# Optimization experiments

Measured on AMD Instinct MI355X. Metric: run time of the kernel, lower is better.

Reference implementation:

```python
import jax, jax.numpy as jnp
import numpy as np

N = 50000
NUM_GRAPHS = 64
EPS = 1e-16  # PyG softmax denominator epsilon


def _gat_conv(x, src, dst, W, a_src, a_dst, b, heads, out_ch):
    n = x.shape[0]
    h = (x @ W).reshape(n, heads, out_ch)                    # [N,H,C]
    al_s = jnp.einsum('nhc,hc->nh', h, a_src)                # [N,H]
    al_d = jnp.einsum('nhc,hc->nh', h, a_dst)                # [N,H]
    e = jax.nn.leaky_relu(al_s[src] + al_d[dst], 0.2)        # [E,H]
    emax = jax.ops.segment_max(e, dst, num_segments=n)       # [N,H]
    ee = jnp.exp(e - emax[dst])
    den = jax.ops.segment_sum(ee, dst, num_segments=n)       # [N,H]
    alpha = ee / (den[dst] + EPS)                            # [E,H]
    msg = h[src] * alpha[:, :, None]                         # [E,H,C]
    out = jax.ops.segment_sum(msg, dst, num_segments=n)      # [N,H,C]
    return out.reshape(n, heads * out_ch) + b


def setup_inputs() -> dict:
    key = jax.random.key(0)
    ks = jax.random.split(key, 16)
    E = 250000
    x = jax.random.normal(ks[0], (N, 11), dtype=jnp.float32)
    edge_index = jax.random.randint(ks[1], (2, E), 0, N, dtype=jnp.int64)
    batch = jnp.sort(jax.random.randint(ks[2], (N,), 0, NUM_GRAPHS, dtype=jnp.int64))
    def glorot(k, shape):
        fan = shape[0] + shape[-1]
        return jax.random.uniform(k, shape, jnp.float32, -1.0, 1.0) * np.sqrt(6.0 / fan)
    return {
        'x': x, 'edge_index': edge_index, 'batch': batch,
        'W1': glorot(ks[3], (11, 8 * 128)),
        'a1s': glorot(ks[4], (8, 128)), 'a1d': glorot(ks[5], (8, 128)),
        'b1': jnp.zeros((8 * 128,), jnp.float32),
        'W2': glorot(ks[6], (1024, 8 * 64)),
        'a2s': glorot(ks[7], (8, 64)), 'a2d': glorot(ks[8], (8, 64)),
        'b2': jnp.zeros((8 * 64,), jnp.float32),
        'W3': glorot(ks[9], (512, 4 * 32)),
        'a3s': glorot(ks[10], (4, 32)), 'a3d': glorot(ks[11], (4, 32)),
        'b3': jnp.zeros((4 * 32,), jnp.float32),
        'Wout': glorot(ks[12], (128, 1)),
        'bout': jnp.zeros((1,), jnp.float32),
    }


def reference(x, edge_index, batch, W1, a1s, a1d, b1, W2, a2s, a2d, b2,
              W3, a3s, a3d, b3, Wout, bout):
    n = x.shape[0]
    # GATConv adds self-loops by default
    loop = jnp.arange(n, dtype=edge_index.dtype)
    src = jnp.concatenate([edge_index[0], loop])
    dst = jnp.concatenate([edge_index[1], loop])
    h = jax.nn.leaky_relu(_gat_conv(x, src, dst, W1, a1s, a1d, b1, 8, 128), 0.01)
    h = jax.nn.leaky_relu(_gat_conv(h, src, dst, W2, a2s, a2d, b2, 8, 64), 0.01)
    h = jax.nn.leaky_relu(_gat_conv(h, src, dst, W3, a3s, a3d, b3, 4, 32), 0.01)
    # global mean pool over graphs
    sums = jax.ops.segment_sum(h, batch, num_segments=NUM_GRAPHS)      # [G,128]
    cnt = jax.ops.segment_sum(jnp.ones((n,), h.dtype), batch, num_segments=NUM_GRAPHS)
    pooled = sums / jnp.maximum(cnt, 1.0)[:, None]
    return pooled @ Wout + bout                                        # [G,1]
```

## Files before the change

### kernel.cpp

```cpp
#include <hip/hip_runtime.h>

#define EPS 1e-16f

typedef __attribute__((ext_vector_type(8))) short short8;
typedef __attribute__((ext_vector_type(4))) float f32x4;

__device__ __forceinline__ float b2f(unsigned short u) {
    return __uint_as_float(((unsigned)u) << 16);
}
__device__ __forceinline__ unsigned short f2b(float f) {
    unsigned u = __float_as_uint(f);
    u += 0x7fffu + ((u >> 16) & 1u);
    return (unsigned short)(u >> 16);
}

typedef __attribute__((address_space(3))) void lds_vp;
typedef __attribute__((address_space(1))) const void glb_vp;
__device__ __forceinline__ void load_lds16(const unsigned short* g,
                                           unsigned short* l) {
    __builtin_amdgcn_global_load_lds((glb_vp*)g, (lds_vp*)l, 16, 0, 0);
}

__global__ void init_deg_kernel(int* deg, int N) {
    int i = blockIdx.x * blockDim.x + threadIdx.x;
    if (i < N) deg[i] = 1;
}

__global__ void hist_kernel(const int* __restrict__ ei, int E, int N, int* deg) {
    int e = blockIdx.x * blockDim.x + threadIdx.x;
    if (e < E) {
        int d = ei[E + e];
        if ((unsigned)d < (unsigned)N) atomicAdd(&deg[d], 1);
    }
}

__global__ void scan_block_kernel(const int* __restrict__ deg,
                                  int* __restrict__ rowst,
                                  int* __restrict__ bsum, int N) {
    __shared__ int s[256];
    int t = threadIdx.x, b = blockIdx.x;
    int i = b * 256 + t;
    s[t] = (i < N) ? deg[i] : 0;
    __syncthreads();
    for (int o = 1; o < 256; o <<= 1) {
        int a = (t >= o) ? s[t - o] : 0;
        __syncthreads();
        s[t] += a;
        __syncthreads();
    }
    if (i < N) rowst[i + 1] = s[t];
    if (t == 255) bsum[b] = s[255];
}

__global__ void scan_top_kernel(const int* __restrict__ bsum,
                                int* __restrict__ boff, int NB) {
    __shared__ int psum[65];
    int t = threadIdx.x;
    int chunk = (NB + 63) / 64;
    int lo = t * chunk, hi = lo + chunk;
    if (lo > NB) lo = NB;
    if (hi > NB) hi = NB;
    int s = 0;
    for (int i = lo; i < hi; i++) s += bsum[i];
    psum[t + 1] = s;
    __syncthreads();
    if (t == 0) {
        psum[0] = 0;
        for (int i = 1; i <= 64; i++) psum[i] += psum[i - 1];
    }
    __syncthreads();
    int run = psum[t];
    for (int i = lo; i < hi; i++) {
        boff[i] = run;
        run += bsum[i];
    }
}

__global__ void scan_add_kernel(int* __restrict__ rowst,
                                const int* __restrict__ boff, int N) {
    int i = blockIdx.x * 256 + threadIdx.x;
    if (i == 0) rowst[0] = 0;
    if (i < N) rowst[i + 1] += boff[blockIdx.x];
}

__global__ void selfloop_kernel(const int* __restrict__ rowst, int* srcs,
                                int* cursor, int N) {
    int n = blockIdx.x * blockDim.x + threadIdx.x;
    if (n < N) {
        srcs[rowst[n]] = n;
        cursor[n] = rowst[n] + 1;
    }
}

__global__ void scatter_kernel(const int* __restrict__ ei, int E, int N,
                               int* cursor, int* srcs) {
    int e = blockIdx.x * blockDim.x + threadIdx.x;
    if (e < E) {
        int d = ei[E + e];
        if ((unsigned)d < (unsigned)N) {
            int p = atomicAdd(&cursor[d], 1);
            int s = ei[e];
            if ((unsigned)s >= (unsigned)N) s = d;
            srcs[p] = s;
        }
    }
}

__global__ void wa1_kernel(const float* __restrict__ W1,
                           const float* __restrict__ a1s,
                           const float* __restrict__ a1d,
                           float* __restrict__ w_as, float* __restrict__ w_ad) {
    int t = threadIdx.x;
    if (t >= 88) return;
    int h = t / 11, k = t % 11;
    float s = 0.f, d = 0.f;
    for (int c = 0; c < 128; c++) {
        float w = W1[k * 1024 + h * 128 + c];
        s += w * a1s[h * 128 + c];
        d += w * a1d[h * 128 + c];
    }
    w_as[h * 16 + k] = s;
    w_ad[h * 16 + k] = d;
}

__global__ void al1_kernel(const float* __restrict__ x,
                           const float* __restrict__ w_as,
                           const float* __restrict__ w_ad,
                           float* __restrict__ als, float* __restrict__ ald,
                           int N) {
    int i = blockIdx.x * blockDim.x + threadIdx.x;
    if (i >= N * 8) return;
    int n = i >> 3, h = i & 7;
    float s = 0.f, d = 0.f;
#pragma unroll
    for (int k = 0; k < 11; k++) {
        float xv = x[n * 11 + k];
        s += xv * w_as[h * 16 + k];
        d += xv * w_ad[h * 16 + k];
    }
    als[i] = s;
    ald[i] = d;
}

__global__ void aggx_kernel(const float* __restrict__ x,
                            const float* __restrict__ escr,
                            const int* __restrict__ rowst,
                            const int* __restrict__ srcs,
                            unsigned short* __restrict__ A2, int N) {
    int n = blockIdx.x;
    int t = threadIdx.x;
    int h = t >> 4, k = t & 15;
    int start = rowst[n], end = rowst[n + 1];
    float acc = 0.f;
    const int CH = 4;
    for (int idx = start; idx < end; idx += CH) {
        int mc = end - idx;
        if (mc > CH) mc = CH;
        int ss[CH];
        float av[CH], xv[CH];
#pragma unroll
        for (int j = 0; j < CH; j++)
            if (j < mc) ss[j] = srcs[idx + j];
#pragma unroll
        for (int j = 0; j < CH; j++)
            if (j < mc) av[j] = escr[(size_t)(idx + j) * 8 + h];
#pragma unroll
        for (int j = 0; j < CH; j++)
            if (j < mc) xv[j] = (k < 11) ? x[ss[j] * 11 + k] : 0.f;
#pragma unroll
        for (int j = 0; j < CH; j++)
            if (j < mc) acc += av[j] * xv[j];
    }
    A2[(size_t)n * 128 + t] = f2b(acc);
}

__global__ void w1bd_kernel(const float* __restrict__ W1,
                            unsigned short* __restrict__ Bt) {
    int i = blockIdx.x * blockDim.x + threadIdx.x;
    if (i >= 1024 * 128) return;
    int n = i >> 7, kk = i & 127;
    int h = kk >> 4, k = kk & 15;
    float v = (h == (n >> 7) && k < 11) ? W1[k * 1024 + n] : 0.f;
    Bt[i] = f2b(v);
}

__global__ void transpose_w_kernel(const float* __restrict__ W,
                                   unsigned short* __restrict__ Wt, int K, int N) {
    int i = blockIdx.x * blockDim.x + threadIdx.x;
    if (i >= K * N) return;
    int k = i / N, n = i % N;
    Wt[(size_t)n * K + k] = f2b(W[i]);
}

template <bool EPI, int HB, int CC>
__global__ __launch_bounds__(256) void gemm_mfma(
    const unsigned short* __restrict__ A, const unsigned short* __restrict__ Bt,
    unsigned short* __restrict__ C, const float* __restrict__ bias,
    const float* __restrict__ a_s, const float* __restrict__ a_d,
    float* __restrict__ als, float* __restrict__ ald, int H, int M, int N,
    int K) {
    int NX = gridDim.x;
    int bid = blockIdx.y * NX + blockIdx.x;
    int win = bid & (8 * NX - 1);
    int mg = bid / (8 * NX);
    int m_t = mg * 8 + (win & 7);
    int n_t = win >> 3;
    int bm = m_t * 128, bn = n_t * 128;
    if (bm >= M) return;

    union SMem {
        struct {
            unsigned short As[2][128 * 32];
            unsigned short Bs[2][128 * 32];
        } k;
        unsigned short Ct[128 * 132];
    };
    __shared__ __align__(16) SMem sm;
    auto& As = sm.k.As;
    auto& Bs = sm.k.Bs;
    auto& Ct = sm.Ct;

    int t = threadIdx.x;
    int w = t >> 6, lane = t & 63;
    int quad = lane >> 4, l16 = lane & 15;
    int wr = (w >> 1) * 64, wc = (w & 1) * 64;

    int c0 = w * 128 + lane;
    int c1 = c0 + 64;
    int r0 = c0 >> 2, p0 = c0 & 3;
    int r1 = c1 >> 2, p1 = c1 & 3;
    int j0 = (p0 - (r0 >> 1)) & 3;
    int j1 = (p1 - (r1 >> 1)) & 3;
    int ga0 = bm + r0;
    if (ga0 >= M) ga0 = M - 1;
    int ga1 = bm + r1;
    if (ga1 >= M) ga1 = M - 1;
    const unsigned short* Ag0 = A + (size_t)ga0 * K + j0 * 8;
    const unsigned short* Ag1 = A + (size_t)ga1 * K + j1 * 8;
    const unsigned short* Bg0 = Bt + (size_t)(bn + r0) * K + j0 * 8;
    const unsigned short* Bg1 = Bt + (size_t)(bn + r1) * K + j1 * 8;

    auto stage = [&](int st, int k0) {
        load_lds16(Ag0 + k0, &As[st][(w * 128) * 8]);
        load_lds16(Ag1 + k0, &As[st][(w * 128 + 64) * 8]);
        load_lds16(Bg0 + k0, &Bs[st][(w * 128) * 8]);
        load_lds16(Bg1 + k0, &Bs[st][(w * 128 + 64) * 8]);
    };

    int aoff[4], boff4[4];
#pragma unroll
    for (int i = 0; i < 4; i++) {
        int ra = wr + i * 16 + l16;
        aoff[i] = ra * 32 + (((quad + (ra >> 1)) & 3) * 8);
        int rb = wc + i * 16 + l16;
        boff4[i] = rb * 32 + (((quad + (rb >> 1)) & 3) * 8);
    }

    f32x4 acc[4][4] = {};
    stage(0, 0);
    int st = 0;
    for (int k0 = 0; k0 < K; k0 += 32, st ^= 1) {
        __syncthreads();
        if (k0 + 32 < K) stage(st ^ 1, k0 + 32);
        short8 a[4], b[4];
#pragma unroll
        for (int mi = 0; mi < 4; mi++) a[mi] = *(const short8*)&As[st][aoff[mi]];
#pragma unroll
        for (int ni = 0; ni < 4; ni++) b[ni] = *(const short8*)&Bs[st][boff4[ni]];
#pragma unroll
        for (int mi = 0; mi < 4; mi++)
#pragma unroll
            for (int ni = 0; ni < 4; ni++)
                acc[mi][ni] = __builtin_amdgcn_mfma_f32_16x16x32_bf16(
                    a[mi], b[ni], acc[mi][ni], 0, 0, 0);
    }
    __syncthreads();

#pragma unroll
    for (int mi = 0; mi < 4; mi++) {
#pragma unroll
        for (int r = 0; r < 4; r++) {
            int rl = wr + mi * 16 + quad * 4 + r;
#pragma unroll
            for (int ni = 0; ni < 4; ni++) {
                int cl = wc + ni * 16 + l16;
                float v = acc[mi][ni][r];
                if (EPI) {
                    v += bias[bn + cl];
                    v = v > 0.f ? v : 0.01f * v;
                }
                Ct[rl * 132 + cl] = f2b(v);
            }
        }
    }
    __syncthreads();
#pragma unroll
    for (int p = 0; p < 16; p++) {
        int q = p * 256 + t;
        int row = q >> 5, c8 = q & 31;
        if (bm + row < M) {
            uint2 v = *(const uint2*)&Ct[row * 132 + c8 * 4];
            *(uint2*)&C[(size_t)(bm + row) * N + bn + c8 * 4] = v;
        }
    }
    if (HB > 0) {
        for (int pi = t; pi < 128 * HB; pi += 256) {
            int row = pi / HB, hl = pi % HB;
            if (bm + row >= M) continue;
            int hg = bn / CC + hl;
            const unsigned short* rp = &Ct[row * 132 + hl * CC];
            const float* asp = a_s + hg * CC;
            const float* adp = a_d + hg * CC;
            float s = 0.f, d = 0.f;
#pragma unroll
            for (int c = 0; c < CC; c++) {
                float v = b2f(rp[c]);
                s += v * asp[c];
                d += v * adp[c];
            }
            als[(size_t)(bm + row) * H + hg] = s;
            ald[(size_t)(bm + row) * H + hg] = d;
        }
    }
}

template <int H>
__global__ void mden_kernel(const float* __restrict__ als,
                            const float* __restrict__ ald,
                            const int* __restrict__ rowst,
                            const int* __restrict__ srcs,
                            float* __restrict__ escr, int N) {
    int i = blockIdx.x * blockDim.x + threadIdx.x;
    if (i >= N * H) return;
    int n = i / H, h = i % H;
    float aldn = ald[i];
    int start = rowst[n], end = rowst[n + 1];
    const int CH = 4;
    float m = -1e30f;
    for (int idx = start; idx < end; idx += CH) {
        int mc = end - idx;
        if (mc > CH) mc = CH;
        int ss[CH];
        float lv[CH];
#pragma unroll
        for (int j = 0; j < CH; j++)
            if (j < mc) ss[j] = srcs[idx + j];
#pragma unroll
        for (int j = 0; j < CH; j++)
            if (j < mc) lv[j] = als[ss[j] * H + h];
#pragma unroll
        for (int j = 0; j < CH; j++)
            if (j < mc) {
                float v = lv[j] + aldn;
                v = v > 0.f ? v : 0.2f * v;
                escr[(size_t)(idx + j) * H + h] = v;
                m = fmaxf(m, v);
            }
    }
    float den = 0.f;
    for (int idx = start; idx < end; idx += CH) {
        int mc = end - idx;
        if (mc > CH) mc = CH;
        float lv[CH];
#pragma unroll
        for (int j = 0; j < CH; j++)
            if (j < mc) lv[j] = escr[(size_t)(idx + j) * H + h];
#pragma unroll
        for (int j = 0; j < CH; j++)
            if (j < mc) den += expf(lv[j] - m);
    }
    float dinv = 1.0f / (den + EPS);
    for (int idx = start; idx < end; idx += CH) {
        int mc = end - idx;
        if (mc > CH) mc = CH;
        float lv[CH];
#pragma unroll
        for (int j = 0; j < CH; j++)
            if (j < mc) lv[j] = escr[(size_t)(idx + j) * H + h];
#pragma unroll
        for (int j = 0; j < CH; j++)
            if (j < mc)
                escr[(size_t)(idx + j) * H + h] = expf(lv[j] - m) * dinv;
    }
}

template <int H, int C>
__global__ void agg_fused4(const unsigned short* __restrict__ hin,
                           const float* __restrict__ als,
                           const float* __restrict__ ald,
                           const int* __restrict__ rowst,
                           const int* __restrict__ srcs,
                           const float* __restrict__ bias,
                           unsigned short* __restrict__ out, int N) {
    constexpr int HC = H * C;
    constexpr int TPH = C / 4;
    int n = blockIdx.x;
    int t = threadIdx.x;
    int c = t * 4;
    int hh = c / C;
    int li = (c % C) / 4;
    int start = rowst[n], end = rowst[n + 1];
    float aldn = ald[n * H + hh];
    float m = -1e30f;
    for (int idx = start + li; idx < end; idx += TPH) {
        float v = als[srcs[idx] * H + hh] + aldn;
        v = v > 0.f ? v : 0.2f * v;
        m = fmaxf(m, v);
    }
#pragma unroll
    for (int o = 1; o < TPH; o <<= 1) m = fmaxf(m, __shfl_xor(m, o));
    float den = 0.f;
    for (int idx = start + li; idx < end; idx += TPH) {
        float v = als[srcs[idx] * H + hh] + aldn;
        v = v > 0.f ? v : 0.2f * v;
        den += expf(v - m);
    }
#pragma unroll
    for (int o = 1; o < TPH; o <<= 1) den += __shfl_xor(den, o);
    float dinv = 1.0f / (den + EPS);

    float a0 = 0.f, a1 = 0.f, a2 = 0.f, a3 = 0.f;
    const int CH = 4;
    for (int idx = start; idx < end; idx += CH) {
        int mc = end - idx;
        if (mc > CH) mc = CH;
        int ss[CH];
        float lv[CH];
        ushort4 uv[CH];
#pragma unroll
        for (int j = 0; j < CH; j++)
            if (j < mc) ss[j] = srcs[idx + j];
#pragma unroll
        for (int j = 0; j < CH; j++)
            if (j < mc) lv[j] = als[ss[j] * H + hh];
#pragma unroll
        for (int j = 0; j < CH; j++)
            if (j < mc) uv[j] = *(const ushort4*)(hin + (size_t)ss[j] * HC + c);
#pragma unroll
        for (int j = 0; j < CH; j++)
            if (j < mc) {
                float v = lv[j] + aldn;
                v = v > 0.f ? v : 0.2f * v;
                float a = expf(v - m) * dinv;
                a0 += a * b2f(uv[j].x);
                a1 += a * b2f(uv[j].y);
                a2 += a * b2f(uv[j].z);
                a3 += a * b2f(uv[j].w);
            }
    }
    float v0 = a0 + bias[c], v1 = a1 + bias[c + 1];
    float v2 = a2 + bias[c + 2], v3 = a3 + bias[c + 3];
    ushort4 o;
    o.x = f2b(v0 > 0.f ? v0 : 0.01f * v0);
    o.y = f2b(v1 > 0.f ? v1 : 0.01f * v1);
    o.z = f2b(v2 > 0.f ? v2 : 0.01f * v2);
    o.w = f2b(v3 > 0.f ? v3 : 0.01f * v3);
    *(ushort4*)&out[(size_t)n * HC + c] = o;
}

template <int H, int C>
__global__ void agg_fused2(const unsigned short* __restrict__ hin,
                           const float* __restrict__ als,
                           const float* __restrict__ ald,
                           const int* __restrict__ rowst,
                           const int* __restrict__ srcs,
                           const float* __restrict__ bias,
                           unsigned short* __restrict__ out, int N) {
    constexpr int HC = H * C;
    constexpr int TPH = C / 2;
    int n = blockIdx.x;
    int t = threadIdx.x;
    int c = t * 2;
    int hh = c / C;
    int li = (c % C) / 2;
    int start = rowst[n], end = rowst[n + 1];
    float aldn = ald[n * H + hh];
    float m = -1e30f;
    for (int idx = start + li; idx < end; idx += TPH) {
        float v = als[srcs[idx] * H + hh] + aldn;
        v = v > 0.f ? v : 0.2f * v;
        m = fmaxf(m, v);
    }
#pragma unroll
    for (int o = 1; o < TPH; o <<= 1) m = fmaxf(m, __shfl_xor(m, o));
    float den = 0.f;
    for (int idx = start + li; idx < end; idx += TPH) {
        float v = als[srcs[idx] * H + hh] + aldn;
        v = v > 0.f ? v : 0.2f * v;
        den += expf(v - m);
    }
#pragma unroll
    for (int o = 1; o < TPH; o <<= 1) den += __shfl_xor(den, o);
    float dinv = 1.0f / (den + EPS);

    float a0 = 0.f, a1 = 0.f;
    const int CH = 4;
    for (int idx = start; idx < end; idx += CH) {
        int mc = end - idx;
        if (mc > CH) mc = CH;
        int ss[CH];
        float lv[CH];
        ushort2 uv[CH];
#pragma unroll
        for (int j = 0; j < CH; j++)
            if (j < mc) ss[j] = srcs[idx + j];
#pragma unroll
        for (int j = 0; j < CH; j++)
            if (j < mc) lv[j] = als[ss[j] * H + hh];
#pragma unroll
        for (int j = 0; j < CH; j++)
            if (j < mc) uv[j] = *(const ushort2*)(hin + (size_t)ss[j] * HC + c);
#pragma unroll
        for (int j = 0; j < CH; j++)
            if (j < mc) {
                float v = lv[j] + aldn;
                v = v > 0.f ? v : 0.2f * v;
                float a = expf(v - m) * dinv;
                a0 += a * b2f(uv[j].x);
                a1 += a * b2f(uv[j].y);
            }
    }
    float v0 = a0 + bias[c], v1 = a1 + bias[c + 1];
    ushort2 o;
    o.x = f2b(v0 > 0.f ? v0 : 0.01f * v0);
    o.y = f2b(v1 > 0.f ? v1 : 0.01f * v1);
    *(ushort2*)&out[(size_t)n * HC + c] = o;
}

__global__ void pool_init_kernel(float* pool, int GC) {
    int i = blockIdx.x * blockDim.x + threadIdx.x;
    if (i < GC) pool[i] = 0.f;
}

__global__ void pool_partial_kernel(const unsigned short* __restrict__ h3,
                                    const int* __restrict__ batch,
                                    float* __restrict__ pool, int N, int G) {
    int lo = blockIdx.x * 128;
    int hi = lo + 128;
    if (hi > N) hi = N;
    if (lo >= N) return;
    int t = threadIdx.x;
    int cur = batch[lo];
    float acc = 0.f;
    for (int n = lo; n < hi; n++) {
        int g = batch[n];
        if (g != cur) {
            if ((unsigned)cur < (unsigned)G) atomicAdd(&pool[cur * 128 + t], acc);
            acc = 0.f;
            cur = g;
        }
        acc += b2f(h3[(size_t)n * 128 + t]);
    }
    if ((unsigned)cur < (unsigned)G) atomicAdd(&pool[cur * 128 + t], acc);
}

__global__ void head_kernel(const float* __restrict__ pool,
                            const int* __restrict__ batch,
                            const float* __restrict__ Wout,
                            const float* __restrict__ bout,
                            float* __restrict__ out, int N) {
    int g = blockIdx.x;
    int t = threadIdx.x;
    int lo, hi;
    {
        int a = 0, b = N;
        while (a < b) { int mid = (a + b) >> 1; if (batch[mid] < g) a = mid + 1; else b = mid; }
        lo = a;
        a = lo; b = N;
        while (a < b) { int mid = (a + b) >> 1; if (batch[mid] < g + 1) a = mid + 1; else b = mid; }
        hi = a;
    }
    float c = (float)(hi - lo);
    c = c > 1.f ? c : 1.f;
    float v = (pool[g * 128 + t] / c) * Wout[t];
    for (int o = 32; o; o >>= 1) v += __shfl_xor(v, o);
    __shared__ float partial[2];
    if ((t & 63) == 0) partial[t >> 6] = v;
    __syncthreads();
    if (t == 0) out[g] = partial[0] + partial[1] + bout[0];
}

extern "C" void kernel_launch(void* const* d_in, const int* in_sizes, int n_in,
                              void* d_out, int out_size, void* d_ws,
                              size_t ws_size, hipStream_t stream) {
    const float* x = (const float*)d_in[0];
    const int* ei = (const int*)d_in[1];
    const int* batch = (const int*)d_in[2];
    const float* W1 = (const float*)d_in[3];
    const float* a1s = (const float*)d_in[4];
    const float* a1d = (const float*)d_in[5];
    const float* b1 = (const float*)d_in[6];
    const float* W2 = (const float*)d_in[7];
    const float* a2s = (const float*)d_in[8];
    const float* a2d = (const float*)d_in[9];
    const float* b2 = (const float*)d_in[10];
    const float* W3 = (const float*)d_in[11];
    const float* a3s = (const float*)d_in[12];
    const float* a3d = (const float*)d_in[13];
    const float* b3 = (const float*)d_in[14];
    const float* Wout = (const float*)d_in[15];
    const float* bout = (const float*)d_in[16];
    float* out = (float*)d_out;

    const int N = in_sizes[0] / 11;
    const int E = in_sizes[1] / 2;
    const int Etot = E + N;
    const int G = out_size;
    const int NB = (N + 255) / 256;
    const int MT = ((N + 127) / 128 + 7) / 8 * 8;

    char* ws = (char*)d_ws;
    size_t off = 0;
    auto alloc = [&](size_t bytes) -> void* {
        void* p = ws + off;
        off += (bytes + 255) & ~(size_t)255;
        return p;
    };
    unsigned short* buf1 = (unsigned short*)alloc((size_t)N * 1024 * 2);
    unsigned short* buf2 = (unsigned short*)alloc((size_t)N * 1024 * 2);
    float* als = (float*)alloc((size_t)N * 8 * 4);
    float* ald = (float*)alloc((size_t)N * 8 * 4);
    float* escr = (float*)alloc((size_t)Etot * 8 * 4);
    int* rowst = (int*)alloc((size_t)(N + 1) * 4);
    int* cursor = (int*)alloc((size_t)N * 4);
    int* srcs = (int*)alloc((size_t)Etot * 4);
    int* deg = (int*)alloc((size_t)N * 4);
    int* bsum = (int*)alloc((size_t)NB * 4);
    int* boff = (int*)alloc((size_t)NB * 4);
    float* pool = (float*)alloc((size_t)G * 128 * 4);
    unsigned short* aggx = (unsigned short*)alloc((size_t)N * 128 * 2);
    unsigned short* w1bd = (unsigned short*)alloc((size_t)1024 * 128 * 2);
    unsigned short* wt2 = (unsigned short*)alloc((size_t)1024 * 512 * 2);
    unsigned short* wt3 = (unsigned short*)alloc((size_t)512 * 128 * 2);
    float* w_as = (float*)alloc(8 * 16 * 4);
    float* w_ad = (float*)alloc(8 * 16 * 4);

    int nb = (N + 255) / 256;
    int eb = (E + 255) / 256;

    init_deg_kernel<<<nb, 256, 0, stream>>>(deg, N);
    hist_kernel<<<eb, 256, 0, stream>>>(ei, E, N, deg);
    scan_block_kernel<<<NB, 256, 0, stream>>>(deg, rowst, bsum, N);
    scan_top_kernel<<<1, 64, 0, stream>>>(bsum, boff, NB);
    scan_add_kernel<<<NB, 256, 0, stream>>>(rowst, boff, N);
    selfloop_kernel<<<nb, 256, 0, stream>>>(rowst, srcs, cursor, N);
    scatter_kernel<<<eb, 256, 0, stream>>>(ei, E, N, cursor, srcs);

    wa1_kernel<<<1, 128, 0, stream>>>(W1, a1s, a1d, w_as, w_ad);
    w1bd_kernel<<<(1024 * 128 + 255) / 256, 256, 0, stream>>>(W1, w1bd);
    transpose_w_kernel<<<(1024 * 512 + 255) / 256, 256, 0, stream>>>(W2, wt2,
                                                                     1024, 512);
    transpose_w_kernel<<<(512 * 128 + 255) / 256, 256, 0, stream>>>(W3, wt3,
                                                                    512, 128);

    al1_kernel<<<(N * 8 + 255) / 256, 256, 0, stream>>>(x, w_as, w_ad, als, ald,
                                                        N);
    mden_kernel<8><<<(N * 8 + 255) / 256, 256, 0, stream>>>(als, ald, rowst,
                                                            srcs, escr, N);
    aggx_kernel<<<N, 128, 0, stream>>>(x, escr, rowst, srcs, aggx, N);
    gemm_mfma<true, 0, 1><<<dim3(8, MT), 256, 0, stream>>>(
        aggx, w1bd, buf2, b1, nullptr, nullptr, nullptr, nullptr, 0, N, 1024,
        128);

    gemm_mfma<false, 2, 64><<<dim3(4, MT), 256, 0, stream>>>(
        buf2, wt2, buf1, nullptr, a2s, a2d, als, ald, 8, N, 512, 1024);
    agg_fused4<8, 64><<<N, 128, 0, stream>>>(buf1, als, ald, rowst, srcs, b2,
                                             buf2, N);

    gemm_mfma<false, 4, 32><<<dim3(1, MT), 256, 0, stream>>>(
        buf2, wt3, buf1, nullptr, a3s, a3d, als, ald, 4, N, 128, 512);
    agg_fused2<4, 32><<<N, 64, 0, stream>>>(buf1, als, ald, rowst, srcs, b3,
                                            buf2, N);

    pool_init_kernel<<<(G * 128 + 255) / 256, 256, 0, stream>>>(pool, G * 128);
    pool_partial_kernel<<<(N + 127) / 128, 128, 0, stream>>>(buf2, batch, pool,
                                                             N, G);
    head_kernel<<<G, 128, 0, stream>>>(pool, batch, Wout, bout, out, N);
}
```

Measured before the change: 491.6 us.

## Fuse preprocessing kernels and exploit block-diagonal W1 to shrink layer-1 GEMM K

After: 512.3 us. +4.2%, slower.

```diff
diff --git a/kernel.cpp b/kernel.cpp
--- a/kernel.cpp
+++ b/kernel.cpp
@@ -76,19 +76,19 @@
     }
 }
 
-__global__ void scan_add_kernel(int* __restrict__ rowst,
-                                const int* __restrict__ boff, int N) {
+__global__ void scan_finish_kernel(int* __restrict__ rowst,
+                                   const int* __restrict__ boff,
+                                   const int* __restrict__ deg,
+                                   int* __restrict__ srcs,
+                                   int* __restrict__ cursor, int N) {
     int i = blockIdx.x * 256 + threadIdx.x;
     if (i == 0) rowst[0] = 0;
-    if (i < N) rowst[i + 1] += boff[blockIdx.x];
-}
-
-__global__ void selfloop_kernel(const int* __restrict__ rowst, int* srcs,
-                                int* cursor, int N) {
-    int n = blockIdx.x * blockDim.x + threadIdx.x;
-    if (n < N) {
-        srcs[rowst[n]] = n;
-        cursor[n] = rowst[n] + 1;
+    if (i < N) {
+        int incl = rowst[i + 1] + boff[blockIdx.x];
+        rowst[i + 1] = incl;
+        int st = incl - deg[i];
+        srcs[st] = i;
+        cursor[i] = st + 1;
     }
 }
 
@@ -106,44 +106,69 @@
     }
 }
 
-__global__ void wa1_kernel(const float* __restrict__ W1,
+__global__ void wprep_kernel(const float* __restrict__ W1,
+                             const float* __restrict__ W2,
+                             const float* __restrict__ W3,
+                             unsigned short* __restrict__ wt2,
+                             unsigned short* __restrict__ wt3,
+                             unsigned short* __restrict__ w1sk) {
+    int i = blockIdx.x * blockDim.x + threadIdx.x;
+    if (i < 1024 * 512) {
+        int k = i / 512, n = i % 512;
+        wt2[(size_t)n * 1024 + k] = f2b(W2[i]);
+    } else if (i < 1024 * 512 + 512 * 128) {
+        int j = i - 1024 * 512;
+        int k = j / 128, n = j % 128;
+        wt3[(size_t)n * 512 + k] = f2b(W3[j]);
+    } else if (i < 1024 * 512 + 512 * 128 + 8 * 128 * 32) {
+        int q = i - (1024 * 512 + 512 * 128);
+        int h = q >> 12, rem = q & 4095;
+        int c = rem >> 5, kk = rem & 31;
+        int off = (h == 7) ? 16 : 0;
+        float v = 0.f;
+        int k = kk - off;
+        if (k >= 0 && k < 11) v = W1[k * 1024 + h * 128 + c];
+        w1sk[q] = f2b(v);
+    }
+}
+
+__global__ void al1_kernel(const float* __restrict__ x,
+                           const float* __restrict__ W1,
                            const float* __restrict__ a1s,
                            const float* __restrict__ a1d,
-                           float* __restrict__ w_as, float* __restrict__ w_ad) {
-    int t = threadIdx.x;
-    if (t >= 88) return;
-    int h = t / 11, k = t % 11;
-    float s = 0.f, d = 0.f;
-    for (int c = 0; c < 128; c++) {
-        float w = W1[k * 1024 + h * 128 + c];
-        s += w * a1s[h * 128 + c];
-        d += w * a1d[h * 128 + c];
-    }
-    w_as[h * 16 + k] = s;
-    w_ad[h * 16 + k] = d;
-}
-
-__global__ void al1_kernel(const float* __restrict__ x,
-                           const float* __restrict__ w_as,
-                           const float* __restrict__ w_ad,
                            float* __restrict__ als, float* __restrict__ ald,
                            int N) {
-    int i = blockIdx.x * blockDim.x + threadIdx.x;
+    __shared__ float was[128], wad[128];
+    int t = threadIdx.x;
+    if (t < 88) {
+        int h = t / 11, k = t % 11;
+        float s = 0.f, d = 0.f;
+        for (int c = 0; c < 128; c++) {
+            float w = W1[k * 1024 + h * 128 + c];
+            s += w * a1s[h * 128 + c];
+            d += w * a1d[h * 128 + c];
+        }
+        was[h * 16 + k] = s;
+        wad[h * 16 + k] = d;
+    }
+    __syncthreads();
+    int i = blockIdx.x * 256 + t;
     if (i >= N * 8) return;
     int n = i >> 3, h = i & 7;
     float s = 0.f, d = 0.f;
 #pragma unroll
     for (int k = 0; k < 11; k++) {
         float xv = x[n * 11 + k];
-        s += xv * w_as[h * 16 + k];
-        d += xv * w_ad[h * 16 + k];
+        s += xv * was[h * 16 + k];
+        d += xv * wad[h * 16 + k];
     }
     als[i] = s;
     ald[i] = d;
 }
 
 __global__ void aggx_kernel(const float* __restrict__ x,
-                            const float* __restrict__ escr,
+                            const float* __restrict__ als,
+                            const float* __restrict__ ald,
                             const int* __restrict__ rowst,
                             const int* __restrict__ srcs,
                             unsigned short* __restrict__ A2, int N) {
@@ -151,54 +176,59 @@
     int t = threadIdx.x;
     int h = t >> 4, k = t & 15;
     int start = rowst[n], end = rowst[n + 1];
+    float aldn = ald[n * 8 + h];
+    float m = -1e30f;
+    for (int idx = start + k; idx < end; idx += 16) {
+        float v = als[srcs[idx] * 8 + h] + aldn;
+        v = v > 0.f ? v : 0.2f * v;
+        m = fmaxf(m, v);
+    }
+#pragma unroll
+    for (int o = 1; o < 16; o <<= 1) m = fmaxf(m, __shfl_xor(m, o));
+    float den = 0.f;
+    for (int idx = start + k; idx < end; idx += 16) {
+        float v = als[srcs[idx] * 8 + h] + aldn;
+        v = v > 0.f ? v : 0.2f * v;
+        den += expf(v - m);
+    }
+#pragma unroll
+    for (int o = 1; o < 16; o <<= 1) den += __shfl_xor(den, o);
+    float dinv = 1.0f / (den + EPS);
+
     float acc = 0.f;
     const int CH = 4;
     for (int idx = start; idx < end; idx += CH) {
         int mc = end - idx;
         if (mc > CH) mc = CH;
         int ss[CH];
-        float av[CH], xv[CH];
+        float lv[CH], xv[CH];
 #pragma unroll
         for (int j = 0; j < CH; j++)
             if (j < mc) ss[j] = srcs[idx + j];
 #pragma unroll
         for (int j = 0; j < CH; j++)
-            if (j < mc) av[j] = escr[(size_t)(idx + j) * 8 + h];
+            if (j < mc) lv[j] = als[ss[j] * 8 + h];
 #pragma unroll
         for (int j = 0; j < CH; j++)
             if (j < mc) xv[j] = (k < 11) ? x[ss[j] * 11 + k] : 0.f;
 #pragma unroll
         for (int j = 0; j < CH; j++)
-            if (j < mc) acc += av[j] * xv[j];
+            if (j < mc) {
+                float v = lv[j] + aldn;
+                v = v > 0.f ? v : 0.2f * v;
+                acc += expf(v - m) * dinv * xv[j];
+            }
     }
     A2[(size_t)n * 128 + t] = f2b(acc);
 }
 
-__global__ void w1bd_kernel(const float* __restrict__ W1,
-                            unsigned short* __restrict__ Bt) {
-    int i = blockIdx.x * blockDim.x + threadIdx.x;
-    if (i >= 1024 * 128) return;
-    int n = i >> 7, kk = i & 127;
-    int h = kk >> 4, k = kk & 15;
-    float v = (h == (n >> 7) && k < 11) ? W1[k * 1024 + n] : 0.f;
-    Bt[i] = f2b(v);
-}
-
-__global__ void transpose_w_kernel(const float* __restrict__ W,
-                                   unsigned short* __restrict__ Wt, int K, int N) {
-    int i = blockIdx.x * blockDim.x + threadIdx.x;
-    if (i >= K * N) return;
-    int k = i / N, n = i % N;
-    Wt[(size_t)n * K + k] = f2b(W[i]);
-}
-
-template <bool EPI, int HB, int CC>
+template <bool EPI, int HB, int CC, bool SK>
 __global__ __launch_bounds__(256) void gemm_mfma(
     const unsigned short* __restrict__ A, const unsigned short* __restrict__ Bt,
     unsigned short* __restrict__ C, const float* __restrict__ bias,
     const float* __restrict__ a_s, const float* __restrict__ a_d,
     float* __restrict__ als, float* __restrict__ ald, int H, int M, int N,
-    int K) {
+    int K, int lda) {
     int NX = gridDim.x;
     int bid = blockIdx.y * NX + blockIdx.x;
     int win = bid & (8 * NX - 1);
@@ -225,6 +255,14 @@
     int quad = lane >> 4, l16 = lane & 15;
     int wr = (w >> 1) * 64, wc = (w & 1) * 64;
 
+    int kofs = 0;
+    const unsigned short* Bb = Bt;
+    if (SK) {
+        kofs = n_t * 16;
+        if (kofs > lda - 32) kofs = lda - 32;
+        Bb = Bt + (size_t)n_t * 128 * 32;
+    }
+
     int c0 = w * 128 + lane;
     int c1 = c0 + 64;
     int r0 = c0 >> 2, p0 = c0 & 3;
@@ -235,10 +273,12 @@
     if (ga0 >= M) ga0 = M - 1;
     int ga1 = bm + r1;
     if (ga1 >= M) ga1 = M - 1;
-    const unsigned short* Ag0 = A + (size_t)ga0 * K + j0 * 8;
-    const unsigned short* Ag1 = A + (size_t)ga1 * K + j1 * 8;
-    const unsigned short* Bg0 = Bt + (size_t)(bn + r0) * K + j0 * 8;
-    const unsigned short* Bg1 = Bt + (size_t)(bn + r1) * K + j1 * 8;
+    const unsigned short* Ag0 = A + (size_t)ga0 * lda + kofs + j0 * 8;
+    const unsigned short* Ag1 = A + (size_t)ga1 * lda + kofs + j1 * 8;
+    size_t br0 = SK ? (size_t)r0 : (size_t)(bn + r0);
+    size_t br1 = SK ? (size_t)r1 : (size_t)(bn + r1);
+    const unsigned short* Bg0 = Bb + br0 * K + j0 * 8;
+    const unsigned short* Bg1 = Bb + br1 * K + j1 * 8;
 
     auto stage = [&](int st, int k0) {
         load_lds16(Ag0 + k0, &As[st][(w * 128) * 8]);
@@ -321,66 +361,6 @@
             als[(size_t)(bm + row) * H + hg] = s;
             ald[(size_t)(bm + row) * H + hg] = d;
         }
-    }
-}
-
-template <int H>
-__global__ void mden_kernel(const float* __restrict__ als,
-                            const float* __restrict__ ald,
-                            const int* __restrict__ rowst,
-                            const int* __restrict__ srcs,
-                            float* __restrict__ escr, int N) {
-    int i = blockIdx.x * blockDim.x + threadIdx.x;
-    if (i >= N * H) return;
-    int n = i / H, h = i % H;
-    float aldn = ald[i];
-    int start = rowst[n], end = rowst[n + 1];
-    const int CH = 4;
-    float m = -1e30f;
-    for (int idx = start; idx < end; idx += CH) {
-        int mc = end - idx;
-        if (mc > CH) mc = CH;
-        int ss[CH];
-        float lv[CH];
-#pragma unroll
-        for (int j = 0; j < CH; j++)
-            if (j < mc) ss[j] = srcs[idx + j];
-#pragma unroll
-        for (int j = 0; j < CH; j++)
-            if (j < mc) lv[j] = als[ss[j] * H + h];
-#pragma unroll
-        for (int j = 0; j < CH; j++)
-            if (j < mc) {
-                float v = lv[j] + aldn;
-                v = v > 0.f ? v : 0.2f * v;
-                escr[(size_t)(idx + j) * H + h] = v;
-                m = fmaxf(m, v);
-            }
-    }
-    float den = 0.f;
-    for (int idx = start; idx < end; idx += CH) {
-        int mc = end - idx;
-        if (mc > CH) mc = CH;
-        float lv[CH];
-#pragma unroll
-        for (int j = 0; j < CH; j++)
-            if (j < mc) lv[j] = escr[(size_t)(idx + j) * H + h];
-#pragma unroll
-        for (int j = 0; j < CH; j++)
-            if (j < mc) den += expf(lv[j] - m);
-    }
-    float dinv = 1.0f / (den + EPS);
-    for (int idx = start; idx < end; idx += CH) {
-        int mc = end - idx;
-        if (mc > CH) mc = CH;
-        float lv[CH];
-#pragma unroll
-        for (int j = 0; j < CH; j++)
-            if (j < mc) lv[j] = escr[(size_t)(idx + j) * H + h];
-#pragma unroll
-        for (int j = 0; j < CH; j++)
-            if (j < mc)
-                escr[(size_t)(idx + j) * H + h] = expf(lv[j] - m) * dinv;
     }
 }
 
@@ -620,7 +600,6 @@
     unsigned short* buf2 = (unsigned short*)alloc((size_t)N * 1024 * 2);
     float* als = (float*)alloc((size_t)N * 8 * 4);
     float* ald = (float*)alloc((size_t)N * 8 * 4);
-    float* escr = (float*)alloc((size_t)Etot * 8 * 4);
     int* rowst = (int*)alloc((size_t)(N + 1) * 4);
     int* cursor = (int*)alloc((size_t)N * 4);
     int* srcs = (int*)alloc((size_t)Etot * 4);
@@ -629,11 +608,9 @@
     int* boff = (int*)alloc((size_t)NB * 4);
     float* pool = (float*)alloc((size_t)G * 128 * 4);
     unsigned short* aggx = (unsigned short*)alloc((size_t)N * 128 * 2);
-    unsigned short* w1bd = (unsigned short*)alloc((size_t)1024 * 128 * 2);
+    unsigned short* w1sk = (unsigned short*)alloc((size_t)8 * 128 * 32 * 2);
     unsigned short* wt2 = (unsigned short*)alloc((size_t)1024 * 512 * 2);
     unsigned short* wt3 = (unsigned short*)alloc((size_t)512 * 128 * 2);
-    float* w_as = (float*)alloc(8 * 16 * 4);
-    float* w_ad = (float*)alloc(8 * 16 * 4);
 
     int nb = (N + 255) / 256;
     int eb = (E + 255) / 256;
@@ -642,33 +619,28 @@
     hist_kernel<<<eb, 256, 0, stream>>>(ei, E, N, deg);
     scan_block_kernel<<<NB, 256, 0, stream>>>(deg, rowst, bsum, N);
     scan_top_kernel<<<1, 64, 0, stream>>>(bsum, boff, NB);
-    scan_add_kernel<<<NB, 256, 0, stream>>>(rowst, boff, N);
-    selfloop_kernel<<<nb, 256, 0, stream>>>(rowst, srcs, cursor, N);
+    scan_finish_kernel<<<NB, 256, 0, stream>>>(rowst, boff, deg, srcs, cursor,
+                                               N);
     scatter_kernel<<<eb, 256, 0, stream>>>(ei, E, N, cursor, srcs);
 
-    wa1_kernel<<<1, 128, 0, stream>>>(W1, a1s, a1d, w_as, w_ad);
-    w1bd_kernel<<<(1024 * 128 + 255) / 256, 256, 0, stream>>>(W1, w1bd);
-    transpose_w_kernel<<<(1024 * 512 + 255) / 256, 256, 0, stream>>>(W2, wt2,
-                                                                     1024, 512);
-    transpose_w_kernel<<<(512 * 128 + 255) / 256, 256, 0, stream>>>(W3, wt3,
-                                                                    512, 128);
-
-    al1_kernel<<<(N * 8 + 255) / 256, 256, 0, stream>>>(x, w_as, w_ad, als, ald,
-                                                        N);
-    mden_kernel<8><<<(N * 8 + 255) / 256, 256, 0, stream>>>(als, ald, rowst,
-                                                            srcs, escr, N);
-    aggx_kernel<<<N, 128, 0, stream>>>(x, escr, rowst, srcs, aggx, N);
-    gemm_mfma<true, 0, 1><<<dim3(8, MT), 256, 0, stream>>>(
-        aggx, w1bd, buf2, b1, nullptr, nullptr, nullptr, nullptr, 0, N, 1024,
-        128);
-
-    gemm_mfma<false, 2, 64><<<dim3(4, MT), 256, 0, stream>>>(
-        buf2, wt2, buf1, nullptr, a2s, a2d, als, ald, 8, N, 512, 1024);
+    const int WTOT = 1024 * 512 + 512 * 128 + 8 * 128 * 32;
+    wprep_kernel<<<(WTOT + 255) / 256, 256, 0, stream>>>(W1, W2, W3, wt2, wt3,
+                                                         w1sk);
+
+    al1_kernel<<<(N * 8 + 255) / 256, 256, 0, stream>>>(x, W1, a1s, a1d, als,
+                                                        ald, N);
+    aggx_kernel<<<N, 128, 0, stream>>>(x, als, ald, rowst, srcs, aggx, N);
+    gemm_mfma<true, 0, 1, true><<<dim3(8, MT), 256, 0, stream>>>(
+        aggx, w1sk, buf2, b1, nullptr, nullptr, nullptr, nullptr, 0, N, 1024,
+        32, 128);
+
+    gemm_mfma<false, 2, 64, false><<<dim3(4, MT), 256, 0, stream>>>(
+        buf2, wt2, buf1, nullptr, a2s, a2d, als, ald, 8, N, 512, 1024, 1024);
     agg_fused4<8, 64><<<N, 128, 0, stream>>>(buf1, als, ald, rowst, srcs, b2,
                                              buf2, N);
 
-    gemm_mfma<false, 4, 32><<<dim3(1, MT), 256, 0, stream>>>(
-        buf2, wt3, buf1, nullptr, a3s, a3d, als, ald, 4, N, 128, 512);
+    gemm_mfma<false, 4, 32, false><<<dim3(1, MT), 256, 0, stream>>>(
+        buf2, wt3, buf1, nullptr, a3s, a3d, als, ald, 4, N, 128, 512, 512);
     agg_fused2<4, 32><<<N, 64, 0, stream>>>(buf1, als, ald, rowst, srcs, b3,
                                             buf2, N);
 
```
